# Kernel optimization log

Hardware: AMD Instinct MI355X
Metric: run time of the kernel (lower is better)

## Reference

```python
import jax, jax.numpy as jnp
import numpy as np

B, N, K = 2, 1024, 16
D_MODEL, D_ELLIP, N_HEADS = 768, 128, 8
NF = D_MODEL // 6            # sinusoidal freqs per coordinate
MAX_LOG_FREQ = 7.0
ENC_H = max(1, N_HEADS // 2) # ellipsoid encoder heads
ENC_FF = 2048                # torch TransformerEncoderLayer default dim_feedforward


def setup_inputs() -> dict:
    key = jax.random.key(0)
    ks = jax.random.split(key, 20)
    rn = lambda k, sh, sc=1.0: jax.random.normal(k, sh, dtype=jnp.float32) * sc
    w = lambda k, o, i: rn(k, (o, i), 1.0 / np.sqrt(i))
    inp = {}
    inp['s'] = rn(ks[0], (B, N, D_MODEL))
    inp['R'] = rn(ks[1], (B, N, 3, 3))
    inp['t'] = rn(ks[2], (B, N, 3))
    inp['ellip_tokens'] = rn(ks[3], (B, K, D_ELLIP))
    inp['mu'] = rn(ks[4], (B, K, 3))
    inp['Sigma'] = rn(ks[5], (B, K, 3, 3))
    inp['ellip_mask'] = jnp.ones((B, K), dtype=jnp.bool_)
    # main attention params (torch Linear convention: [out, in])
    inp['mix_w'] = w(ks[6], 6 * NF, 6 * NF)
    inp['lin_cov_w'] = w(ks[7], D_MODEL, 9)
    inp['q_w'] = w(ks[8], D_MODEL, D_MODEL)
    inp['k_w'] = w(ks[9], D_MODEL, 2 * D_MODEL)
    inp['v_w'] = w(ks[10], D_MODEL, D_MODEL + D_ELLIP)
    inp['o_w'] = w(ks[11], D_MODEL, D_MODEL)
    # ellipsoid TransformerEncoderLayer params (post-norm, eval mode)
    inp['enc_in_w'] = w(ks[12], 3 * D_ELLIP, D_ELLIP)
    inp['enc_in_b'] = jnp.zeros((3 * D_ELLIP,), jnp.float32)
    inp['enc_out_w'] = w(ks[13], D_ELLIP, D_ELLIP)
    inp['enc_out_b'] = jnp.zeros((D_ELLIP,), jnp.float32)
    inp['lin1_w'] = w(ks[14], ENC_FF, D_ELLIP)
    inp['lin1_b'] = jnp.zeros((ENC_FF,), jnp.float32)
    inp['lin2_w'] = w(ks[15], D_ELLIP, ENC_FF)
    inp['lin2_b'] = jnp.zeros((D_ELLIP,), jnp.float32)
    inp['ln1_g'] = jnp.ones((D_ELLIP,), jnp.float32)
    inp['ln1_b'] = jnp.zeros((D_ELLIP,), jnp.float32)
    inp['ln2_g'] = jnp.ones((D_ELLIP,), jnp.float32)
    inp['ln2_b'] = jnp.zeros((D_ELLIP,), jnp.float32)
    return inp


def _layernorm(x, g, b, eps=1e-5):
    m = x.mean(-1, keepdims=True)
    v = ((x - m) ** 2).mean(-1, keepdims=True)
    return (x - m) / jnp.sqrt(v + eps) * g + b


def _fwd(s, R, t, ellip_tokens, mu, Sigma, mix_w, lin_cov_w, q_w, k_w, v_w, o_w,
         enc_in_w, enc_in_b, enc_out_w, enc_out_b, lin1_w, lin1_b, lin2_w, lin2_b,
         ln1_g, ln1_b, ln2_g, ln2_b, ellip_mask):
    # --- ellipsoid self-attn encoder (single post-norm layer, eval mode) ---
    x = ellip_tokens                                   # [B,K,de]
    qkv = x @ enc_in_w.T + enc_in_b
    q, kk, v = jnp.split(qkv, 3, axis=-1)
    dhe = D_ELLIP // ENC_H
    qh = q.reshape(B, K, ENC_H, dhe)
    kh = kk.reshape(B, K, ENC_H, dhe)
    vh = v.reshape(B, K, ENC_H, dhe)
    sc = jnp.einsum('bqhd,bkhd->bhqk', qh, kh) / np.sqrt(dhe).astype(np.float32)
    ao = jnp.einsum('bhqk,bkhd->bqhd', jax.nn.softmax(sc, -1), vh).reshape(B, K, D_ELLIP)
    ao = ao @ enc_out_w.T + enc_out_b
    x = _layernorm(x + ao, ln1_g, ln1_b)
    ff = jax.nn.relu(x @ lin1_w.T + lin1_b) @ lin2_w.T + lin2_b
    e = _layernorm(x + ff, ln2_g, ln2_b)               # [B,K,de]
    # --- per-query local frame transforms ---
    diff = mu[:, None, :, :] - t[:, :, None, :]        # [B,N,K,3]
    r = jnp.einsum('bnji,bnkj->bnki', R, diff)         # R^T @ diff
    C = jnp.einsum('bnji,bkjl,bnlm->bnkim', R, Sigma, R)  # R^T Sigma R [B,N,K,3,3]
    # --- sinusoidal posenc (sin first, then cos; flatten coord-major) ---
    freqs = 2.0 ** jnp.linspace(0.0, MAX_LOG_FREQ, NF).astype(jnp.float32)
    xf = r[..., None] * freqs                          # [B,N,K,3,NF]
    feat = jnp.concatenate([jnp.sin(xf), jnp.cos(xf)], axis=-2).reshape(B, N, K, 6 * NF)
    pos = feat @ mix_w.T                               # [B,N,K,d]
    cov = C.reshape(B, N, K, 9) @ lin_cov_w.T          # [B,N,K,d]
    K_mat = jnp.concatenate([pos, cov], -1) @ k_w.T    # [B,N,K,d]
    eB = jnp.broadcast_to(e[:, None, :, :], (B, N, K, D_ELLIP))
    V_mat = jnp.concatenate([pos, eB], -1) @ v_w.T     # [B,N,K,d]
    Q = s @ q_w.T                                      # [B,N,d]
    dh = D_MODEL // N_HEADS
    Qh = Q.reshape(B, N, N_HEADS, dh)
    Kh = K_mat.reshape(B, N, K, N_HEADS, dh)
    Vh = V_mat.reshape(B, N, K, N_HEADS, dh)
    scores = jnp.einsum('bnhd,bnkhd->bnhk', Qh, Kh) / np.sqrt(dh).astype(np.float32)
    scores = scores + (1.0 - ellip_mask.astype(scores.dtype))[:, None, None, :] * -10000.0
    attn = jax.nn.softmax(scores, -1)                  # [B,N,H,K]
    out = jnp.einsum('bnhk,bnkhd->bnhd', attn, Vh).reshape(B, N, D_MODEL)
    return out @ o_w.T


def reference(s, R, t, ellip_tokens, mu, Sigma, mix_w, lin_cov_w, q_w, k_w, v_w, o_w,
              enc_in_w, enc_in_b, enc_out_w, enc_out_b, lin1_w, lin1_b, lin2_w, lin2_b,
              ln1_g, ln1_b, ln2_g, ln2_b, ellip_mask):
    return _fwd(s, R, t, ellip_tokens, mu, Sigma, mix_w, lin_cov_w, q_w, k_w, v_w, o_w,
                enc_in_w, enc_in_b, enc_out_w, enc_out_b, lin1_w, lin1_b, lin2_w, lin2_b,
                ln1_g, ln1_b, ln2_g, ln2_b, ellip_mask)
```

## Files before the change

kernel.cpp:

```cpp
#include <hip/hip_runtime.h>
#include <math.h>

#define BB     2
#define SEQ    1024
#define KTOK   16
#define DM     768
#define DE     128
#define NH     8
#define DHD    96
#define EH     4
#define DHE    32
#define EFF    2048

typedef short short8 __attribute__((ext_vector_type(8)));
typedef float f32x4 __attribute__((ext_vector_type(4)));
typedef unsigned short ushort_t;

__device__ __forceinline__ void split2(float x, ushort_t& h, ushort_t& l) {
  unsigned u = __float_as_uint(x);
  unsigned hb = (u + 0x7fffu + ((u >> 16) & 1u)) >> 16;
  float hf = __uint_as_float(hb << 16);
  float r = x - hf;
  unsigned u2 = __float_as_uint(r);
  unsigned lb = (u2 + 0x7fffu + ((u2 >> 16) & 1u)) >> 16;
  h = (ushort_t)hb;
  l = (ushort_t)lb;
}

typedef const unsigned int __attribute__((address_space(1)))* gas_p;
typedef unsigned int __attribute__((address_space(3)))* las_p;
__device__ __forceinline__ void load_lds16(const ushort_t* g, ushort_t* l) {
  __builtin_amdgcn_global_load_lds((gas_p)g, (las_p)l, 16, 0, 0);
}

__global__ __launch_bounds__(256) void split_all(
    const float* __restrict__ s, const float* __restrict__ q_w,
    const float* __restrict__ o_w, const float* __restrict__ k_w,
    const float* __restrict__ v_w,
    ushort_t* __restrict__ sS, ushort_t* __restrict__ qwS,
    ushort_t* __restrict__ owS, ushort_t* __restrict__ kwS,
    ushort_t* __restrict__ vwS)
{
  int z = blockIdx.y;
  const float* in; int ldin; ushort_t* out; int rows;
  switch (z) {
    case 0: in = s;   ldin = DM;      out = sS;  rows = BB * SEQ; break;
    case 1: in = q_w; ldin = DM;      out = qwS; rows = DM; break;
    case 2: in = o_w; ldin = DM;      out = owS; rows = DM; break;
    case 3: in = k_w; ldin = 2 * DM;  out = kwS; rows = DM; break;
    default: in = v_w; ldin = DM + DE; out = vwS; rows = DM; break;
  }
  long i = (long)blockIdx.x * 256 + threadIdx.x;
  const int perRow = DM >> 2;
  if (i >= (long)rows * perRow) return;
  int r = (int)(i / perRow), c4 = (int)(i % perRow) << 2;
  float4 v = *(const float4*)(in + (long)r * ldin + c4);
  ushort_t h[4], l[4];
  split2(v.x, h[0], l[0]);
  split2(v.y, h[1], l[1]);
  split2(v.z, h[2], l[2]);
  split2(v.w, h[3], l[3]);
  ushort_t* orow = out + (long)r * 1536;
  ushort4 hv; hv.x = h[0]; hv.y = h[1]; hv.z = h[2]; hv.w = h[3];
  ushort4 lv; lv.x = l[0]; lv.y = l[1]; lv.z = l[2]; lv.w = l[3];
  *(ushort4*)(orow + c4) = hv;
  *(ushort4*)(orow + DM + c4) = lv;
}

__global__ __launch_bounds__(256) void transpose_split(
    const float* __restrict__ in, int ldin, ushort_t* __restrict__ out,
    int K, int N)
{
  __shared__ float tile[64][65];
  int n0 = blockIdx.x * 64, k0 = blockIdx.y * 64;
  int tid = threadIdx.x;
  #pragma unroll
  for (int p = 0; p < 16; p++) {
    int idx = p * 256 + tid;
    int rr = idx >> 6, cc = idx & 63;
    tile[rr][cc] = in[(long)(k0 + rr) * ldin + n0 + cc];
  }
  __syncthreads();
  #pragma unroll
  for (int p = 0; p < 16; p++) {
    int idx = p * 256 + tid;
    int nr = idx >> 6, kc = idx & 63;
    ushort_t h, l;
    split2(tile[kc][nr], h, l);
    out[(long)(n0 + nr) * 2 * K + (k0 + kc)] = h;
    out[(long)(n0 + nr) * 2 * K + K + (k0 + kc)] = l;
  }
}

template<int OMODE, bool ADD>
__global__ __launch_bounds__(256) void gemm3t(
    const ushort_t* __restrict__ A, int lda, int aKstep, int aLoOff,
    const ushort_t* __restrict__ B, long bOffZ, int ldb, int bKstep, int bLoOff,
    void* __restrict__ Cv, int ldc, int cOffZ, int cLoOff,
    const float* __restrict__ addv, int ldadd, int addOffZ,
    int M, int N, int K)
{
  int z = blockIdx.z;
  B += (long)z * bOffZ;
  int aC0 = z * aKstep, bC0 = z * bKstep;
  const int row0 = blockIdx.y * 64, col0 = blockIdx.x * 64;
  __shared__ ushort_t Ah[2][2048], Al[2][2048], Bh[2][2048], Bl[2][2048];
  int tid = threadIdx.x;
  int wave = tid >> 6, lane = tid & 63;
  int quad = lane >> 4, mrow = lane & 15;
  int wm = (wave >> 1) * 32, wn = (wave & 1) * 32;
  int sr = tid >> 2, q8 = (tid & 3) << 3;
  int wbase = wave << 9;
  f32x4 acc[2][2] = {};

  const ushort_t* pa = A + (long)(row0 + sr) * lda + (aC0 + q8);
  const ushort_t* pb = B + (long)(col0 + sr) * ldb + (bC0 + q8);

  load_lds16(pa, &Ah[0][wbase]);
  load_lds16(pa + aLoOff, &Al[0][wbase]);
  load_lds16(pb, &Bh[0][wbase]);
  load_lds16(pb + bLoOff, &Bl[0][wbase]);

  int buf = 0;
  for (int k0 = 0; k0 < K; k0 += 32) {
    __syncthreads();
    if (k0 + 32 < K) {
      int kn = k0 + 32;
      load_lds16(pa + kn, &Ah[buf ^ 1][wbase]);
      load_lds16(pa + aLoOff + kn, &Al[buf ^ 1][wbase]);
      load_lds16(pb + kn, &Bh[buf ^ 1][wbase]);
      load_lds16(pb + bLoOff + kn, &Bl[buf ^ 1][wbase]);
    }
    short8 fah[2], fal[2], fbh[2], fbl[2];
    #pragma unroll
    for (int t = 0; t < 2; t++) {
      fah[t] = *(const short8*)&Ah[buf][(wm + t * 16 + mrow) * 32 + (quad << 3)];
      fal[t] = *(const short8*)&Al[buf][(wm + t * 16 + mrow) * 32 + (quad << 3)];
      fbh[t] = *(const short8*)&Bh[buf][(wn + t * 16 + mrow) * 32 + (quad << 3)];
      fbl[t] = *(const short8*)&Bl[buf][(wn + t * 16 + mrow) * 32 + (quad << 3)];
    }
    #pragma unroll
    for (int mt = 0; mt < 2; mt++)
      #pragma unroll
      for (int nt = 0; nt < 2; nt++) {
        f32x4 c = acc[mt][nt];
        c = __builtin_amdgcn_mfma_f32_16x16x32_bf16(fah[mt], fbh[nt], c, 0, 0, 0);
        c = __builtin_amdgcn_mfma_f32_16x16x32_bf16(fal[mt], fbh[nt], c, 0, 0, 0);
        c = __builtin_amdgcn_mfma_f32_16x16x32_bf16(fah[mt], fbl[nt], c, 0, 0, 0);
        acc[mt][nt] = c;
      }
    buf ^= 1;
  }
  float* Cf = (float*)Cv + (long)z * cOffZ;
  ushort_t* Cs = (ushort_t*)Cv + (long)z * cOffZ;
  const float* av = ADD ? (addv + (long)z * addOffZ) : nullptr;
  #pragma unroll
  for (int mt = 0; mt < 2; mt++)
    #pragma unroll
    for (int nt = 0; nt < 2; nt++) {
      int col = col0 + wn + nt * 16 + mrow;
      if (col >= N) continue;
      int rb = row0 + wm + mt * 16 + (quad << 2);
      #pragma unroll
      for (int rr = 0; rr < 4; rr++) {
        float v = acc[mt][nt][rr];
        if (ADD) v += av[(long)(rb + rr) * ldadd + col];
        if (OMODE == 0) {
          Cf[(long)(rb + rr) * ldc + col] = v;
        } else {
          ushort_t h, l;
          split2(v, h, l);
          Cs[(long)(rb + rr) * ldc + col] = h;
          Cs[(long)(rb + rr) * ldc + cLoOff + col] = l;
        }
      }
    }
}

__global__ __launch_bounds__(256) void bk9_kernel(
    const float* __restrict__ k_w, const float* __restrict__ lin_cov,
    float* __restrict__ Bk9)
{
  int idx = blockIdx.x * 256 + threadIdx.x;
  if (idx >= DM * 9) return;
  int r = idx / 9, p = idx % 9;
  const float* kr = k_w + (long)r * (2 * DM) + DM;
  float acc = 0.f;
  for (int j = 0; j < DM; j++) acc = fmaf(kr[j], lin_cov[j * 9 + p], acc);
  Bk9[idx] = acc;
}

__global__ __launch_bounds__(256) void qb_kernel(
    const ushort_t* __restrict__ QS, const float* __restrict__ Bk9,
    float* __restrict__ QB)
{
  int idx = blockIdx.x * 256 + threadIdx.x;
  if (idx >= BB * SEQ * NH * 9) return;
  int bn = idx / 72, rem = idx % 72, h = rem / 9, p = rem % 9;
  const ushort_t* qr = QS + (long)bn * 1536 + h * DHD;
  float acc = 0.f;
  for (int k = 0; k < DHD; k++) {
    float q = __uint_as_float((unsigned)qr[k] << 16) +
              __uint_as_float((unsigned)qr[DM + k] << 16);
    acc = fmaf(q, Bk9[(h * DHD + k) * 9 + p], acc);
  }
  QB[idx] = acc;
}

__global__ __launch_bounds__(128) void enc_qkv(
    const float* __restrict__ tok, const float* __restrict__ w,
    const float* __restrict__ bias, float* __restrict__ qkv)
{
  int tkn = blockIdx.y;
  int o = blockIdx.x * 128 + threadIdx.x;
  __shared__ float xr[DE];
  int tid = threadIdx.x;
  xr[tid] = tok[tkn * DE + tid];
  __syncthreads();
  float acc = bias[o];
  const float4* wr = (const float4*)(w + (long)o * DE);
  #pragma unroll 8
  for (int j = 0; j < DE / 4; j++) {
    float4 p = wr[j];
    acc = fmaf(p.x, xr[j * 4 + 0], acc);
    acc = fmaf(p.y, xr[j * 4 + 1], acc);
    acc = fmaf(p.z, xr[j * 4 + 2], acc);
    acc = fmaf(p.w, xr[j * 4 + 3], acc);
  }
  qkv[tkn * 384 + o] = acc;
}

__global__ __launch_bounds__(128) void enc_attn_ln1(
    const float* __restrict__ tok, const float* __restrict__ qkvG,
    const float* __restrict__ out_w, const float* __restrict__ out_b,
    const float* __restrict__ ln1_g, const float* __restrict__ ln1_b,
    float* __restrict__ x1G)
{
  int idx = blockIdx.x;
  int b = idx >> 4, tk = idx & 15;
  int tid = threadIdx.x;
  __shared__ float qkvs[KTOK][384];
  __shared__ float ao[DE];
  __shared__ float scl[EH][KTOK], attnl[EH][KTOK];
  __shared__ float red[2];
  __shared__ float stats[2];
  for (int i = tid; i < KTOK * 384; i += 128)
    qkvs[i / 384][i % 384] = qkvG[b * KTOK * 384 + i];
  __syncthreads();
  if (tid < EH * KTOK) {
    int h = tid >> 4, kk = tid & 15;
    float acc = 0.f;
    #pragma unroll 8
    for (int d = 0; d < DHE; d++)
      acc = fmaf(qkvs[tk][h * DHE + d], qkvs[kk][DE + h * DHE + d], acc);
    scl[h][kk] = acc * 0.17677669529663687f;
  }
  __syncthreads();
  if (tid < EH) {
    float m = -1e30f;
    for (int kk = 0; kk < KTOK; kk++) m = fmaxf(m, scl[tid][kk]);
    float s = 0.f;
    for (int kk = 0; kk < KTOK; kk++) { float e = expf(scl[tid][kk] - m); attnl[tid][kk] = e; s += e; }
    float inv = 1.f / s;
    for (int kk = 0; kk < KTOK; kk++) attnl[tid][kk] *= inv;
  }
  __syncthreads();
  {
    int h = tid / DHE;
    float acc = 0.f;
    #pragma unroll
    for (int kk = 0; kk < KTOK; kk++) acc = fmaf(attnl[h][kk], qkvs[kk][256 + tid], acc);
    ao[tid] = acc;
  }
  __syncthreads();
  float val;
  {
    float acc = out_b[tid];
    const float4* wr = (const float4*)(out_w + (long)tid * DE);
    #pragma unroll 8
    for (int j = 0; j < DE / 4; j++) {
      float4 p = wr[j];
      acc = fmaf(p.x, ao[j * 4 + 0], acc);
      acc = fmaf(p.y, ao[j * 4 + 1], acc);
      acc = fmaf(p.z, ao[j * 4 + 2], acc);
      acc = fmaf(p.w, ao[j * 4 + 3], acc);
    }
    val = tok[idx * DE + tid] + acc;
  }
  {
    float v = val;
    #pragma unroll
    for (int off = 32; off > 0; off >>= 1) v += __shfl_down(v, off);
    if ((tid & 63) == 0) red[tid >> 6] = v;
    __syncthreads();
    if (tid == 0) stats[0] = (red[0] + red[1]) * (1.f / DE);
    __syncthreads();
    float d = val - stats[0];
    float v2 = d * d;
    #pragma unroll
    for (int off = 32; off > 0; off >>= 1) v2 += __shfl_down(v2, off);
    if ((tid & 63) == 0) red[tid >> 6] = v2;
    __syncthreads();
    if (tid == 0) stats[1] = rsqrtf((red[0] + red[1]) * (1.f / DE) + 1e-5f);
    __syncthreads();
    x1G[idx * DE + tid] = (val - stats[0]) * stats[1] * ln1_g[tid] + ln1_b[tid];
  }
}

__global__ __launch_bounds__(256) void enc_ff1(
    const float* __restrict__ x1G, const float* __restrict__ lin1_w,
    const float* __restrict__ lin1_b, float* __restrict__ ff1G)
{
  int tkn = blockIdx.x >> 3;
  int f = ((blockIdx.x & 7) << 8) + threadIdx.x;
  __shared__ float xs[DE];
  if (threadIdx.x < DE) xs[threadIdx.x] = x1G[tkn * DE + threadIdx.x];
  __syncthreads();
  float acc = lin1_b[f];
  const float4* wr = (const float4*)(lin1_w + (long)f * DE);
  #pragma unroll 8
  for (int j = 0; j < DE / 4; j++) {
    float4 p = wr[j];
    acc = fmaf(p.x, xs[j * 4 + 0], acc);
    acc = fmaf(p.y, xs[j * 4 + 1], acc);
    acc = fmaf(p.z, xs[j * 4 + 2], acc);
    acc = fmaf(p.w, xs[j * 4 + 3], acc);
  }
  ff1G[tkn * EFF + f] = fmaxf(acc, 0.f);
}

__global__ __launch_bounds__(256) void enc_ff2(
    const float* __restrict__ x1G, const float* __restrict__ ff1G,
    const float* __restrict__ lin2_w, const float* __restrict__ lin2_b,
    float* __restrict__ tmp2G)
{
  int wv = (blockIdx.x << 2) + (threadIdx.x >> 6);
  int tkn = wv >> 7, j = wv & 127;
  int lane = threadIdx.x & 63;
  const float* wr = lin2_w + (long)j * EFF;
  const float* fr = ff1G + (long)tkn * EFF;
  float acc = 0.f;
  #pragma unroll 8
  for (int i = 0; i < EFF / 64; i++) {
    int p = (i << 6) + lane;
    acc = fmaf(wr[p], fr[p], acc);
  }
  #pragma unroll
  for (int off = 32; off > 0; off >>= 1) acc += __shfl_down(acc, off);
  if (lane == 0)
    tmp2G[tkn * DE + j] = x1G[tkn * DE + j] + lin2_b[j] + acc;
}

__global__ __launch_bounds__(256) void enc_ln2_evec(
    const float* __restrict__ tmp2G, const float* __restrict__ ln2_g,
    const float* __restrict__ ln2_b, const float* __restrict__ v_w,
    float* __restrict__ evec)
{
  int idx = blockIdx.x;
  int tid = threadIdx.x;
  __shared__ float el[DE];
  __shared__ float red[4];
  __shared__ float stats[2];
  float val = (tid < DE) ? tmp2G[idx * DE + tid] : 0.f;
  {
    float v = val;
    #pragma unroll
    for (int off = 32; off > 0; off >>= 1) v += __shfl_down(v, off);
    if ((tid & 63) == 0) red[tid >> 6] = v;
    __syncthreads();
    if (tid == 0) stats[0] = (red[0] + red[1] + red[2] + red[3]) * (1.f / DE);
    __syncthreads();
    float d = (tid < DE) ? (val - stats[0]) : 0.f;
    float v2 = d * d;
    #pragma unroll
    for (int off = 32; off > 0; off >>= 1) v2 += __shfl_down(v2, off);
    if ((tid & 63) == 0) red[tid >> 6] = v2;
    __syncthreads();
    if (tid == 0) stats[1] = rsqrtf((red[0] + red[1] + red[2] + red[3]) * (1.f / DE) + 1e-5f);
    __syncthreads();
    if (tid < DE) el[tid] = (val - stats[0]) * stats[1] * ln2_g[tid] + ln2_b[tid];
    __syncthreads();
  }
  #pragma unroll
  for (int r = 0; r < 3; r++) {
    int d = tid + (r << 8);
    float acc = 0.f;
    const float4* wr = (const float4*)(v_w + (long)d * (DM + DE) + DM);
    #pragma unroll 8
    for (int j = 0; j < DE / 4; j++) {
      float4 p = wr[j];
      acc = fmaf(p.x, el[j * 4 + 0], acc);
      acc = fmaf(p.y, el[j * 4 + 1], acc);
      acc = fmaf(p.z, el[j * 4 + 2], acc);
      acc = fmaf(p.w, el[j * 4 + 3], acc);
    }
    evec[idx * DM + d] = acc;
  }
}

__global__ __launch_bounds__(256) void main_attn(
    const float* __restrict__ Rg, const float* __restrict__ tg,
    const float* __restrict__ mug, const float* __restrict__ Sigg,
    const float* __restrict__ QAg, const float* __restrict__ QBg,
    const float* __restrict__ evec, ushort_t* __restrict__ wfeatS,
    float* __restrict__ outeG)
{
  int bn = blockIdx.x;
  int b = bn >> 10;
  int tid = threadIdx.x;
  int w = tid >> 6, lane = tid & 63;
  int h0 = w * 2, h1 = w * 2 + 1;
  __shared__ float Rm[9], tm[3];
  __shared__ float rK[KTOK][3];
  __shared__ float C9[KTOK][9];
  __shared__ float featL[KTOK][772];
  __shared__ float QBl[NH][12];
  __shared__ float scl[NH][KTOK];
  __shared__ float attnl[NH][KTOK];
  __shared__ float freqsL[128];
  float qa0[12], qa1[12];
  {
    const float* qbase = QAg + (long)bn * (NH * DM);
    #pragma unroll
    for (int i = 0; i < 12; i++) {
      qa0[i] = qbase[h0 * DM + i * 64 + lane];
      qa1[i] = qbase[h1 * DM + i * 64 + lane];
    }
  }
  if (tid < 9) Rm[tid] = Rg[bn * 9 + tid];
  if (tid >= 16 && tid < 19) tm[tid - 16] = tg[bn * 3 + (tid - 16)];
  if (tid >= 32 && tid < 32 + NH * 9) {
    int q = tid - 32;
    QBl[q / 9][q % 9] = QBg[bn * (NH * 9) + q];
  }
  if (tid >= 128 && tid < 256) {
    const float step = 7.0f / 127.0f;
    freqsL[tid - 128] = exp2f(step * (float)(tid - 128));
  }
  __syncthreads();
  if (tid < KTOK) {
    int k = tid;
    float diff[3];
    #pragma unroll
    for (int j = 0; j < 3; j++) diff[j] = mug[(b * KTOK + k) * 3 + j] - tm[j];
    #pragma unroll
    for (int i = 0; i < 3; i++) {
      float a = 0.f;
      #pragma unroll
      for (int j = 0; j < 3; j++) a = fmaf(Rm[j * 3 + i], diff[j], a);
      rK[k][i] = a;
    }
    float SR[9];
    const float* Sg = Sigg + (b * KTOK + k) * 9;
    #pragma unroll
    for (int j = 0; j < 3; j++)
      #pragma unroll
      for (int m2 = 0; m2 < 3; m2++) {
        float a = 0.f;
        #pragma unroll
        for (int l = 0; l < 3; l++) a = fmaf(Sg[j * 3 + l], Rm[l * 3 + m2], a);
        SR[j * 3 + m2] = a;
      }
    #pragma unroll
    for (int i = 0; i < 3; i++)
      #pragma unroll
      for (int m2 = 0; m2 < 3; m2++) {
        float a = 0.f;
        #pragma unroll
        for (int j = 0; j < 3; j++) a = fmaf(Rm[j * 3 + i], SR[j * 3 + m2], a);
        C9[k][i * 3 + m2] = a;
      }
  }
  __syncthreads();
  for (int i = tid; i < KTOK * 384; i += 256) {
    int k = i / 384, jj = i % 384;
    int coord = jj >> 7, f = jj & 127;
    float xf = rK[k][coord] * freqsL[f];
    float sv, cv;
    __sincosf(xf, &sv, &cv);
    featL[k][jj] = sv;
    featL[k][jj + 384] = cv;
  }
  __syncthreads();
  for (int k = 0; k < KTOK; k++) {
    float a0 = 0.f, a1 = 0.f;
    #pragma unroll
    for (int i = 0; i < 12; i++) {
      float fv = featL[k][i * 64 + lane];
      a0 = fmaf(qa0[i], fv, a0);
      a1 = fmaf(qa1[i], fv, a1);
    }
    #pragma unroll
    for (int off = 32; off > 0; off >>= 1) {
      a0 += __shfl_down(a0, off);
      a1 += __shfl_down(a1, off);
    }
    if (lane == 0) { scl[h0][k] = a0; scl[h1][k] = a1; }
  }
  __syncthreads();
  if (tid < NH) {
    int h = tid;
    float vals[KTOK];
    float m = -1e30f;
    for (int k = 0; k < KTOK; k++) {
      float a = scl[h][k];
      #pragma unroll
      for (int p = 0; p < 9; p++) a = fmaf(C9[k][p], QBl[h][p], a);
      a *= 0.10206207261596575f;
      vals[k] = a;
      m = fmaxf(m, a);
    }
    float s = 0.f;
    for (int k = 0; k < KTOK; k++) { float e = expf(vals[k] - m); attnl[h][k] = e; s += e; }
    float inv = 1.f / s;
    for (int k = 0; k < KTOK; k++) attnl[h][k] *= inv;
  }
  __syncthreads();
  {
    float at0[KTOK], at1[KTOK];
    #pragma unroll
    for (int k = 0; k < KTOK; k++) { at0[k] = attnl[h0][k]; at1[k] = attnl[h1][k]; }
    ushort_t* wrow = wfeatS + (long)bn * (2 * NH * DM);
    for (int jj = lane; jj < DM; jj += 64) {
      float a0 = 0.f, a1 = 0.f;
      #pragma unroll
      for (int k = 0; k < KTOK; k++) {
        float fv = featL[k][jj];
        a0 = fmaf(at0[k], fv, a0);
        a1 = fmaf(at1[k], fv, a1);
      }
      ushort_t h, l;
      split2(a0, h, l);
      wrow[h0 * DM + jj] = h;
      wrow[NH * DM + h0 * DM + jj] = l;
      split2(a1, h, l);
      wrow[h1 * DM + jj] = h;
      wrow[NH * DM + h1 * DM + jj] = l;
    }
  }
  for (int d = tid; d < DM; d += 256) {
    int h = d / DHD;
    float acc = 0.f;
    #pragma unroll
    for (int k = 0; k < KTOK; k++)
      acc = fmaf(attnl[h][k], evec[(b * KTOK + k) * DM + d], acc);
    outeG[(long)bn * DM + d] = acc;
  }
}

extern "C" void kernel_launch(void* const* d_in, const int* in_sizes, int n_in,
                              void* d_out, int out_size, void* d_ws, size_t ws_size,
                              hipStream_t stream) {
  const float* s    = (const float*)d_in[0];
  const float* R    = (const float*)d_in[1];
  const float* t    = (const float*)d_in[2];
  const float* tok  = (const float*)d_in[3];
  const float* mu   = (const float*)d_in[4];
  const float* Sig  = (const float*)d_in[5];
  const float* mix_w     = (const float*)d_in[7];
  const float* lin_cov_w = (const float*)d_in[8];
  const float* q_w  = (const float*)d_in[9];
  const float* k_w  = (const float*)d_in[10];
  const float* v_w  = (const float*)d_in[11];
  const float* o_w  = (const float*)d_in[12];
  const float* enc_in_w  = (const float*)d_in[13];
  const float* enc_in_b  = (const float*)d_in[14];
  const float* enc_out_w = (const float*)d_in[15];
  const float* enc_out_b = (const float*)d_in[16];
  const float* lin1_w = (const float*)d_in[17];
  const float* lin1_b = (const float*)d_in[18];
  const float* lin2_w = (const float*)d_in[19];
  const float* lin2_b = (const float*)d_in[20];
  const float* ln1_g = (const float*)d_in[21];
  const float* ln1_b = (const float*)d_in[22];
  const float* ln2_g = (const float*)d_in[23];
  const float* ln2_b = (const float*)d_in[24];
  float* out = (float*)d_out;
  char* wsb  = (char*)d_ws;

  const int BN = BB * SEQ;
  float* qkv  = (float*)(wsb);
  float* x1e  = (float*)(wsb + 49152);
  float* ff1e = (float*)(wsb + 65536);
  float* t2e  = (float*)(wsb + 327680);
  float* evec = (float*)(wsb + 344064);
  float* Bk9  = (float*)(wsb + 442368);
  char* p = wsb + 470016;
  ushort_t* qwS   = (ushort_t*)p;  p += 2359296;
  ushort_t* owS   = (ushort_t*)p;  p += 2359296;
  ushort_t* kwS   = (ushort_t*)p;  p += 2359296;
  ushort_t* vwS   = (ushort_t*)p;  p += 2359296;
  ushort_t* mixTS = (ushort_t*)p;  p += 2359296;
  ushort_t* AkTS  = (ushort_t*)p;  p += 2359296;
  ushort_t* AvS   = (ushort_t*)p;  p += 2359296;
  ushort_t* sS    = (ushort_t*)p;  p += 6291456;
  ushort_t* QS    = (ushort_t*)p;  p += 6291456;
  float*    QB    = (float*)p;     p += 589824;
  float*    oute  = (float*)p;     p += 6291456;
  float*    QA    = (float*)p;     p += 50331648;
  ushort_t* wfeatS = (ushort_t*)QA;
  ushort_t* US     = sS;

  dim3 blk(256);

  enc_qkv<<<dim3(3, BB * KTOK), dim3(128), 0, stream>>>(tok, enc_in_w, enc_in_b, qkv);
  enc_attn_ln1<<<BB * KTOK, dim3(128), 0, stream>>>(tok, qkv, enc_out_w, enc_out_b,
                                                    ln1_g, ln1_b, x1e);
  enc_ff1<<<256, blk, 0, stream>>>(x1e, lin1_w, lin1_b, ff1e);
  enc_ff2<<<1024, blk, 0, stream>>>(x1e, ff1e, lin2_w, lin2_b, t2e);
  enc_ln2_evec<<<BB * KTOK, blk, 0, stream>>>(t2e, ln2_g, ln2_b, v_w, evec);

  split_all<<<dim3(1536, 5), blk, 0, stream>>>(s, q_w, o_w, k_w, v_w,
                                               sS, qwS, owS, kwS, vwS);
  transpose_split<<<dim3(12, 12), blk, 0, stream>>>(mix_w, DM, mixTS, DM, DM);
  bk9_kernel<<<27, blk, 0, stream>>>(k_w, lin_cov_w, Bk9);

  gemm3t<1, false><<<dim3(12, 12, 1), blk, 0, stream>>>(
      mixTS, 1536, 0, DM,  kwS, 0, 1536, 0, DM,
      AkTS, 1536, 0, DM,  nullptr, 0, 0,  DM, DM, DM);
  gemm3t<1, false><<<dim3(12, 12, 1), blk, 0, stream>>>(
      vwS, 1536, 0, DM,  mixTS, 0, 1536, 0, DM,
      AvS, 1536, 0, DM,  nullptr, 0, 0,  DM, DM, DM);
  gemm3t<1, false><<<dim3(12, 32, 1), blk, 0, stream>>>(
      sS, 1536, 0, DM,  qwS, 0, 1536, 0, DM,
      QS, 1536, 0, DM,  nullptr, 0, 0,  BN, DM, DM);
  qb_kernel<<<576, blk, 0, stream>>>(QS, Bk9, QB);
  gemm3t<0, false><<<dim3(12, 32, NH), blk, 0, stream>>>(
      QS, 1536, DHD, DM,  AkTS, 0, 1536, DHD, DM,
      QA, NH * DM, DM, 0,  nullptr, 0, 0,  BN, DM, DHD);

  main_attn<<<BN, blk, 0, stream>>>(R, t, mu, Sig, QA, QB, evec, wfeatS, oute);

  gemm3t<1, true><<<dim3(2, 32, NH), blk, 0, stream>>>(
      wfeatS, 2 * NH * DM, DM, NH * DM,  AvS, (long)DHD * 1536, 1536, 0, DM,
      US, 1536, DHD, DM,  oute, DM, DHD,  BN, DHD, DM);
  gemm3t<0, false><<<dim3(12, 32, 1), blk, 0, stream>>>(
      US, 1536, 0, DM,  owS, 0, 1536, 0, DM,
      out, DM, 0, 0,  nullptr, 0, 0,  BN, DM, DM);
}
```

Measured before the change: 380.5 us.

## Merge independent prep and GEMM kernels into combined launches; halve main_attn feature LDS

```diff
diff --git a/kernel.cpp b/kernel.cpp
--- a/kernel.cpp
+++ b/kernel.cpp
@@ -33,78 +33,16 @@
   __builtin_amdgcn_global_load_lds((gas_p)g, (las_p)l, 16, 0, 0);
 }
 
-__global__ __launch_bounds__(256) void split_all(
-    const float* __restrict__ s, const float* __restrict__ q_w,
-    const float* __restrict__ o_w, const float* __restrict__ k_w,
-    const float* __restrict__ v_w,
-    ushort_t* __restrict__ sS, ushort_t* __restrict__ qwS,
-    ushort_t* __restrict__ owS, ushort_t* __restrict__ kwS,
-    ushort_t* __restrict__ vwS)
-{
-  int z = blockIdx.y;
-  const float* in; int ldin; ushort_t* out; int rows;
-  switch (z) {
-    case 0: in = s;   ldin = DM;      out = sS;  rows = BB * SEQ; break;
-    case 1: in = q_w; ldin = DM;      out = qwS; rows = DM; break;
-    case 2: in = o_w; ldin = DM;      out = owS; rows = DM; break;
-    case 3: in = k_w; ldin = 2 * DM;  out = kwS; rows = DM; break;
-    default: in = v_w; ldin = DM + DE; out = vwS; rows = DM; break;
-  }
-  long i = (long)blockIdx.x * 256 + threadIdx.x;
-  const int perRow = DM >> 2;
-  if (i >= (long)rows * perRow) return;
-  int r = (int)(i / perRow), c4 = (int)(i % perRow) << 2;
-  float4 v = *(const float4*)(in + (long)r * ldin + c4);
-  ushort_t h[4], l[4];
-  split2(v.x, h[0], l[0]);
-  split2(v.y, h[1], l[1]);
-  split2(v.z, h[2], l[2]);
-  split2(v.w, h[3], l[3]);
-  ushort_t* orow = out + (long)r * 1536;
-  ushort4 hv; hv.x = h[0]; hv.y = h[1]; hv.z = h[2]; hv.w = h[3];
-  ushort4 lv; lv.x = l[0]; lv.y = l[1]; lv.z = l[2]; lv.w = l[3];
-  *(ushort4*)(orow + c4) = hv;
-  *(ushort4*)(orow + DM + c4) = lv;
-}
-
-__global__ __launch_bounds__(256) void transpose_split(
-    const float* __restrict__ in, int ldin, ushort_t* __restrict__ out,
-    int K, int N)
-{
-  __shared__ float tile[64][65];
-  int n0 = blockIdx.x * 64, k0 = blockIdx.y * 64;
-  int tid = threadIdx.x;
-  #pragma unroll
-  for (int p = 0; p < 16; p++) {
-    int idx = p * 256 + tid;
-    int rr = idx >> 6, cc = idx & 63;
-    tile[rr][cc] = in[(long)(k0 + rr) * ldin + n0 + cc];
-  }
-  __syncthreads();
-  #pragma unroll
-  for (int p = 0; p < 16; p++) {
-    int idx = p * 256 + tid;
-    int nr = idx >> 6, kc = idx & 63;
-    ushort_t h, l;
-    split2(tile[kc][nr], h, l);
-    out[(long)(n0 + nr) * 2 * K + (k0 + kc)] = h;
-    out[(long)(n0 + nr) * 2 * K + K + (k0 + kc)] = l;
-  }
-}
-
 template<int OMODE, bool ADD>
-__global__ __launch_bounds__(256) void gemm3t(
-    const ushort_t* __restrict__ A, int lda, int aKstep, int aLoOff,
-    const ushort_t* __restrict__ B, long bOffZ, int ldb, int bKstep, int bLoOff,
-    void* __restrict__ Cv, int ldc, int cOffZ, int cLoOff,
-    const float* __restrict__ addv, int ldadd, int addOffZ,
-    int M, int N, int K)
-{
-  int z = blockIdx.z;
-  B += (long)z * bOffZ;
-  int aC0 = z * aKstep, bC0 = z * bKstep;
-  const int row0 = blockIdx.y * 64, col0 = blockIdx.x * 64;
-  __shared__ ushort_t Ah[2][2048], Al[2][2048], Bh[2][2048], Bl[2][2048];
+__device__ __forceinline__ void gemm_body(
+    ushort_t (*AhB)[2048], ushort_t (*AlB)[2048],
+    ushort_t (*BhB)[2048], ushort_t (*BlB)[2048],
+    const ushort_t* A, int lda, int aC0, int aLoOff,
+    const ushort_t* B, int ldb, int bC0, int bLoOff,
+    void* Cv, int ldc, int cLoOff,
+    const float* av, int ldadd,
+    int row0, int col0, int N, int K)
+{
   int tid = threadIdx.x;
   int wave = tid >> 6, lane = tid & 63;
   int quad = lane >> 4, mrow = lane & 15;
@@ -116,28 +54,28 @@
   const ushort_t* pa = A + (long)(row0 + sr) * lda + (aC0 + q8);
   const ushort_t* pb = B + (long)(col0 + sr) * ldb + (bC0 + q8);
 
-  load_lds16(pa, &Ah[0][wbase]);
-  load_lds16(pa + aLoOff, &Al[0][wbase]);
-  load_lds16(pb, &Bh[0][wbase]);
-  load_lds16(pb + bLoOff, &Bl[0][wbase]);
+  load_lds16(pa, &AhB[0][wbase]);
+  load_lds16(pa + aLoOff, &AlB[0][wbase]);
+  load_lds16(pb, &BhB[0][wbase]);
+  load_lds16(pb + bLoOff, &BlB[0][wbase]);
 
   int buf = 0;
   for (int k0 = 0; k0 < K; k0 += 32) {
     __syncthreads();
     if (k0 + 32 < K) {
       int kn = k0 + 32;
-      load_lds16(pa + kn, &Ah[buf ^ 1][wbase]);
-      load_lds16(pa + aLoOff + kn, &Al[buf ^ 1][wbase]);
-      load_lds16(pb + kn, &Bh[buf ^ 1][wbase]);
-      load_lds16(pb + bLoOff + kn, &Bl[buf ^ 1][wbase]);
+      load_lds16(pa + kn, &AhB[buf ^ 1][wbase]);
+      load_lds16(pa + aLoOff + kn, &AlB[buf ^ 1][wbase]);
+      load_lds16(pb + kn, &BhB[buf ^ 1][wbase]);
+      load_lds16(pb + bLoOff + kn, &BlB[buf ^ 1][wbase]);
     }
     short8 fah[2], fal[2], fbh[2], fbl[2];
     #pragma unroll
     for (int t = 0; t < 2; t++) {
-      fah[t] = *(const short8*)&Ah[buf][(wm + t * 16 + mrow) * 32 + (quad << 3)];
-      fal[t] = *(const short8*)&Al[buf][(wm + t * 16 + mrow) * 32 + (quad << 3)];
-      fbh[t] = *(const short8*)&Bh[buf][(wn + t * 16 + mrow) * 32 + (quad << 3)];
-      fbl[t] = *(const short8*)&Bl[buf][(wn + t * 16 + mrow) * 32 + (quad << 3)];
+      fah[t] = *(const short8*)&AhB[buf][(wm + t * 16 + mrow) * 32 + (quad << 3)];
+      fal[t] = *(const short8*)&AlB[buf][(wm + t * 16 + mrow) * 32 + (quad << 3)];
+      fbh[t] = *(const short8*)&BhB[buf][(wn + t * 16 + mrow) * 32 + (quad << 3)];
+      fbl[t] = *(const short8*)&BlB[buf][(wn + t * 16 + mrow) * 32 + (quad << 3)];
     }
     #pragma unroll
     for (int mt = 0; mt < 2; mt++)
@@ -151,9 +89,8 @@
       }
     buf ^= 1;
   }
-  float* Cf = (float*)Cv + (long)z * cOffZ;
-  ushort_t* Cs = (ushort_t*)Cv + (long)z * cOffZ;
-  const float* av = ADD ? (addv + (long)z * addOffZ) : nullptr;
+  float* Cf = (float*)Cv;
+  ushort_t* Cs = (ushort_t*)Cv;
   #pragma unroll
   for (int mt = 0; mt < 2; mt++)
     #pragma unroll
@@ -177,57 +114,202 @@
     }
 }
 
-__global__ __launch_bounds__(256) void bk9_kernel(
-    const float* __restrict__ k_w, const float* __restrict__ lin_cov,
-    float* __restrict__ Bk9)
-{
-  int idx = blockIdx.x * 256 + threadIdx.x;
-  if (idx >= DM * 9) return;
-  int r = idx / 9, p = idx % 9;
-  const float* kr = k_w + (long)r * (2 * DM) + DM;
-  float acc = 0.f;
-  for (int j = 0; j < DM; j++) acc = fmaf(kr[j], lin_cov[j * 9 + p], acc);
-  Bk9[idx] = acc;
-}
-
-__global__ __launch_bounds__(256) void qb_kernel(
-    const ushort_t* __restrict__ QS, const float* __restrict__ Bk9,
+template<int OMODE, bool ADD>
+__global__ __launch_bounds__(256) void gemm3t(
+    const ushort_t* __restrict__ A, int lda, int aKstep, int aLoOff,
+    const ushort_t* __restrict__ B, long bOffZ, int ldb, int bKstep, int bLoOff,
+    void* __restrict__ Cv, int ldc, int cOffZ, int cLoOff,
+    const float* __restrict__ addv, int ldadd, int addOffZ,
+    int M, int N, int K)
+{
+  __shared__ ushort_t Ah[2][2048], Al[2][2048], Bh[2][2048], Bl[2][2048];
+  int z = blockIdx.z;
+  void* Cz = (OMODE == 0) ? (void*)((float*)Cv + (long)z * cOffZ)
+                          : (void*)((ushort_t*)Cv + (long)z * cOffZ);
+  gemm_body<OMODE, ADD>(Ah, Al, Bh, Bl,
+      A, lda, z * aKstep, aLoOff,
+      B + (long)z * bOffZ, ldb, z * bKstep, bLoOff,
+      Cz, ldc, cLoOff,
+      ADD ? addv + (long)z * addOffZ : nullptr, ldadd,
+      blockIdx.y * 64, blockIdx.x * 64, N, K);
+}
+
+__global__ __launch_bounds__(256) void combo1(
+    const float* __restrict__ s, const float* __restrict__ q_w,
+    const float* __restrict__ o_w, const float* __restrict__ k_w,
+    const float* __restrict__ v_w,
+    ushort_t* __restrict__ sS, ushort_t* __restrict__ qwS,
+    ushort_t* __restrict__ owS, ushort_t* __restrict__ kwS,
+    ushort_t* __restrict__ vwS,
+    const float* __restrict__ mix_w, ushort_t* __restrict__ mixTS,
+    const float* __restrict__ tok, const float* __restrict__ enc_in_w,
+    const float* __restrict__ enc_in_b, float* __restrict__ qkv,
+    const float* __restrict__ lin_cov_w, float* __restrict__ Bk9)
+{
+  int r = blockIdx.x, tid = threadIdx.x;
+  if (r < 3840) {
+    const float* in; int ldin; ushort_t* out; int base;
+    if (r < 1536)      { in = s;   ldin = DM;      out = sS;  base = 0; }
+    else if (r < 2112) { in = q_w; ldin = DM;      out = qwS; base = 1536; }
+    else if (r < 2688) { in = o_w; ldin = DM;      out = owS; base = 2112; }
+    else if (r < 3264) { in = k_w; ldin = 2 * DM;  out = kwS; base = 2688; }
+    else               { in = v_w; ldin = DM + DE; out = vwS; base = 3264; }
+    long i = (long)(r - base) * 256 + tid;
+    int rr = (int)(i / 192), c4 = (int)(i % 192) << 2;
+    float4 v = *(const float4*)(in + (long)rr * ldin + c4);
+    ushort_t h[4], l[4];
+    split2(v.x, h[0], l[0]);
+    split2(v.y, h[1], l[1]);
+    split2(v.z, h[2], l[2]);
+    split2(v.w, h[3], l[3]);
+    ushort_t* orow = out + (long)rr * 1536;
+    ushort4 hv; hv.x = h[0]; hv.y = h[1]; hv.z = h[2]; hv.w = h[3];
+    ushort4 lv; lv.x = l[0]; lv.y = l[1]; lv.z = l[2]; lv.w = l[3];
+    *(ushort4*)(orow + c4) = hv;
+    *(ushort4*)(orow + DM + c4) = lv;
+  } else if (r < 3984) {
+    __shared__ float tile[64][65];
+    int idx = r - 3840;
+    int n0 = (idx % 12) * 64, k0 = (idx / 12) * 64;
+    #pragma unroll
+    for (int p = 0; p < 16; p++) {
+      int q = p * 256 + tid;
+      int rr = q >> 6, cc = q & 63;
+      tile[rr][cc] = mix_w[(long)(k0 + rr) * DM + n0 + cc];
+    }
+    __syncthreads();
+    #pragma unroll
+    for (int p = 0; p < 16; p++) {
+      int q = p * 256 + tid;
+      int nr = q >> 6, kc = q & 63;
+      ushort_t h, l;
+      split2(tile[kc][nr], h, l);
+      mixTS[(long)(n0 + nr) * 1536 + (k0 + kc)] = h;
+      mixTS[(long)(n0 + nr) * 1536 + DM + (k0 + kc)] = l;
+    }
+  } else if (r < 4016) {
+    __shared__ float xr[DE];
+    int tkn = r - 3984;
+    if (tid < DE) xr[tid] = tok[tkn * DE + tid];
+    __syncthreads();
+    for (int o = tid; o < 3 * DE; o += 256) {
+      float acc = enc_in_b[o];
+      const float4* wr = (const float4*)(enc_in_w + (long)o * DE);
+      #pragma unroll 8
+      for (int j = 0; j < DE / 4; j++) {
+        float4 p = wr[j];
+        acc = fmaf(p.x, xr[j * 4 + 0], acc);
+        acc = fmaf(p.y, xr[j * 4 + 1], acc);
+        acc = fmaf(p.z, xr[j * 4 + 2], acc);
+        acc = fmaf(p.w, xr[j * 4 + 3], acc);
+      }
+      qkv[tkn * 384 + o] = acc;
+    }
+  } else {
+    int idx = (r - 4016) * 256 + tid;
+    if (idx < DM * 9) {
+      int rr = idx / 9, p = idx % 9;
+      const float* kr = k_w + (long)rr * (2 * DM) + DM;
+      float acc = 0.f;
+      for (int j = 0; j < DM; j++) acc = fmaf(kr[j], lin_cov_w[j * 9 + p], acc);
+      Bk9[idx] = acc;
+    }
+  }
+}
+
+__global__ __launch_bounds__(256) void mega1(
+    const ushort_t* __restrict__ sS, const ushort_t* __restrict__ qwS,
+    const ushort_t* __restrict__ mixTS, const ushort_t* __restrict__ kwS,
+    const ushort_t* __restrict__ vwS,
+    ushort_t* __restrict__ QS, ushort_t* __restrict__ AkTS,
+    ushort_t* __restrict__ AvS,
+    const float* __restrict__ t2e, const float* __restrict__ ln2_g,
+    const float* __restrict__ ln2_b, const float* __restrict__ v_w,
+    float* __restrict__ evec)
+{
+  __shared__ ushort_t Ah[2][2048], Al[2][2048], Bh[2][2048], Bl[2][2048];
+  int r = blockIdx.x, tid = threadIdx.x;
+  if (r < 384) {
+    gemm_body<1, false>(Ah, Al, Bh, Bl, sS, 1536, 0, DM, qwS, 1536, 0, DM,
+                        QS, 1536, DM, nullptr, 0, (r / 12) * 64, (r % 12) * 64, DM, DM);
+  } else if (r < 528) {
+    int t2 = r - 384;
+    gemm_body<1, false>(Ah, Al, Bh, Bl, mixTS, 1536, 0, DM, kwS, 1536, 0, DM,
+                        AkTS, 1536, DM, nullptr, 0, (t2 / 12) * 64, (t2 % 12) * 64, DM, DM);
+  } else if (r < 672) {
+    int t2 = r - 528;
+    gemm_body<1, false>(Ah, Al, Bh, Bl, vwS, 1536, 0, DM, mixTS, 1536, 0, DM,
+                        AvS, 1536, DM, nullptr, 0, (t2 / 12) * 64, (t2 % 12) * 64, DM, DM);
+  } else {
+    __shared__ float el[DE];
+    __shared__ float red[4];
+    __shared__ float stats[2];
+    int idx = r - 672;
+    float val = (tid < DE) ? t2e[idx * DE + tid] : 0.f;
+    {
+      float v = val;
+      #pragma unroll
+      for (int off = 32; off > 0; off >>= 1) v += __shfl_down(v, off);
+      if ((tid & 63) == 0) red[tid >> 6] = v;
+      __syncthreads();
+      if (tid == 0) stats[0] = (red[0] + red[1] + red[2] + red[3]) * (1.f / DE);
+      __syncthreads();
+      float d = (tid < DE) ? (val - stats[0]) : 0.f;
+      float v2 = d * d;
+      #pragma unroll
+      for (int off = 32; off > 0; off >>= 1) v2 += __shfl_down(v2, off);
+      if ((tid & 63) == 0) red[tid >> 6] = v2;
+      __syncthreads();
+      if (tid == 0) stats[1] = rsqrtf((red[0] + red[1] + red[2] + red[3]) * (1.f / DE) + 1e-5f);
+      __syncthreads();
+      if (tid < DE) el[tid] = (val - stats[0]) * stats[1] * ln2_g[tid] + ln2_b[tid];
+      __syncthreads();
+    }
+    #pragma unroll
+    for (int q = 0; q < 3; q++) {
+      int d = tid + (q << 8);
+      float acc = 0.f;
+      const float4* wr = (const float4*)(v_w + (long)d * (DM + DE) + DM);
+      #pragma unroll 8
+      for (int j = 0; j < DE / 4; j++) {
+        float4 p = wr[j];
+        acc = fmaf(p.x, el[j * 4 + 0], acc);
+        acc = fmaf(p.y, el[j * 4 + 1], acc);
+        acc = fmaf(p.z, el[j * 4 + 2], acc);
+        acc = fmaf(p.w, el[j * 4 + 3], acc);
+      }
+      evec[idx * DM + d] = acc;
+    }
+  }
+}
+
+__global__ __launch_bounds__(256) void qa_qb(
+    const ushort_t* __restrict__ QS, const ushort_t* __restrict__ AkTS,
+    float* __restrict__ QA, const float* __restrict__ Bk9,
     float* __restrict__ QB)
 {
-  int idx = blockIdx.x * 256 + threadIdx.x;
-  if (idx >= BB * SEQ * NH * 9) return;
-  int bn = idx / 72, rem = idx % 72, h = rem / 9, p = rem % 9;
-  const ushort_t* qr = QS + (long)bn * 1536 + h * DHD;
-  float acc = 0.f;
-  for (int k = 0; k < DHD; k++) {
-    float q = __uint_as_float((unsigned)qr[k] << 16) +
-              __uint_as_float((unsigned)qr[DM + k] << 16);
-    acc = fmaf(q, Bk9[(h * DHD + k) * 9 + p], acc);
-  }
-  QB[idx] = acc;
-}
-
-__global__ __launch_bounds__(128) void enc_qkv(
-    const float* __restrict__ tok, const float* __restrict__ w,
-    const float* __restrict__ bias, float* __restrict__ qkv)
-{
-  int tkn = blockIdx.y;
-  int o = blockIdx.x * 128 + threadIdx.x;
-  __shared__ float xr[DE];
-  int tid = threadIdx.x;
-  xr[tid] = tok[tkn * DE + tid];
-  __syncthreads();
-  float acc = bias[o];
-  const float4* wr = (const float4*)(w + (long)o * DE);
-  #pragma unroll 8
-  for (int j = 0; j < DE / 4; j++) {
-    float4 p = wr[j];
-    acc = fmaf(p.x, xr[j * 4 + 0], acc);
-    acc = fmaf(p.y, xr[j * 4 + 1], acc);
-    acc = fmaf(p.z, xr[j * 4 + 2], acc);
-    acc = fmaf(p.w, xr[j * 4 + 3], acc);
-  }
-  qkv[tkn * 384 + o] = acc;
+  __shared__ ushort_t Ah[2][2048], Al[2][2048], Bh[2][2048], Bl[2][2048];
+  int r = blockIdx.x;
+  if (r < 3072) {
+    int z = r / 384, rr = r % 384;
+    gemm_body<0, false>(Ah, Al, Bh, Bl,
+        QS, 1536, z * DHD, DM, AkTS, 1536, z * DHD, DM,
+        (void*)(QA + (long)z * DM), NH * DM, 0, nullptr, 0,
+        (rr / 12) * 64, (rr % 12) * 64, DM, DHD);
+  } else {
+    int idx = (r - 3072) * 256 + threadIdx.x;
+    if (idx < BB * SEQ * NH * 9) {
+      int bn = idx / 72, rem = idx % 72, h = rem / 9, p = rem % 9;
+      const ushort_t* qr = QS + (long)bn * 1536 + h * DHD;
+      float acc = 0.f;
+      for (int k = 0; k < DHD; k++) {
+        float q = __uint_as_float((unsigned)qr[k] << 16) +
+                  __uint_as_float((unsigned)qr[DM + k] << 16);
+        acc = fmaf(q, Bk9[(h * DHD + k) * 9 + p], acc);
+      }
+      QB[idx] = acc;
+    }
+  }
 }
 
 __global__ __launch_bounds__(128) void enc_attn_ln1(
@@ -351,53 +433,6 @@
     tmp2G[tkn * DE + j] = x1G[tkn * DE + j] + lin2_b[j] + acc;
 }
 
-__global__ __launch_bounds__(256) void enc_ln2_evec(
-    const float* __restrict__ tmp2G, const float* __restrict__ ln2_g,
-    const float* __restrict__ ln2_b, const float* __restrict__ v_w,
-    float* __restrict__ evec)
-{
-  int idx = blockIdx.x;
-  int tid = threadIdx.x;
-  __shared__ float el[DE];
-  __shared__ float red[4];
-  __shared__ float stats[2];
-  float val = (tid < DE) ? tmp2G[idx * DE + tid] : 0.f;
-  {
-    float v = val;
-    #pragma unroll
-    for (int off = 32; off > 0; off >>= 1) v += __shfl_down(v, off);
-    if ((tid & 63) == 0) red[tid >> 6] = v;
-    __syncthreads();
-    if (tid == 0) stats[0] = (red[0] + red[1] + red[2] + red[3]) * (1.f / DE);
-    __syncthreads();
-    float d = (tid < DE) ? (val - stats[0]) : 0.f;
-    float v2 = d * d;
-    #pragma unroll
-    for (int off = 32; off > 0; off >>= 1) v2 += __shfl_down(v2, off);
-    if ((tid & 63) == 0) red[tid >> 6] = v2;
-    __syncthreads();
-    if (tid == 0) stats[1] = rsqrtf((red[0] + red[1] + red[2] + red[3]) * (1.f / DE) + 1e-5f);
-    __syncthreads();
-    if (tid < DE) el[tid] = (val - stats[0]) * stats[1] * ln2_g[tid] + ln2_b[tid];
-    __syncthreads();
-  }
-  #pragma unroll
-  for (int r = 0; r < 3; r++) {
-    int d = tid + (r << 8);
-    float acc = 0.f;
-    const float4* wr = (const float4*)(v_w + (long)d * (DM + DE) + DM);
-    #pragma unroll 8
-    for (int j = 0; j < DE / 4; j++) {
-      float4 p = wr[j];
-      acc = fmaf(p.x, el[j * 4 + 0], acc);
-      acc = fmaf(p.y, el[j * 4 + 1], acc);
-      acc = fmaf(p.z, el[j * 4 + 2], acc);
-      acc = fmaf(p.w, el[j * 4 + 3], acc);
-    }
-    evec[idx * DM + d] = acc;
-  }
-}
-
 __global__ __launch_bounds__(256) void main_attn(
     const float* __restrict__ Rg, const float* __restrict__ tg,
     const float* __restrict__ mug, const float* __restrict__ Sigg,
@@ -409,11 +444,11 @@
   int b = bn >> 10;
   int tid = threadIdx.x;
   int w = tid >> 6, lane = tid & 63;
-  int h0 = w * 2, h1 = w * 2 + 1;
+  int h0 = 2 * w, h1 = 2 * w + 1;
   __shared__ float Rm[9], tm[3];
   __shared__ float rK[KTOK][3];
   __shared__ float C9[KTOK][9];
-  __shared__ float featL[KTOK][772];
+  __shared__ float featL[8][772];
   __shared__ float QBl[NH][12];
   __shared__ float scl[NH][KTOK];
   __shared__ float attnl[NH][KTOK];
@@ -433,7 +468,7 @@
     int q = tid - 32;
     QBl[q / 9][q % 9] = QBg[bn * (NH * 9) + q];
   }
-  if (tid >= 128 && tid < 256) {
+  if (tid >= 128) {
     const float step = 7.0f / 127.0f;
     freqsL[tid - 128] = exp2f(step * (float)(tid - 128));
   }
@@ -472,32 +507,34 @@
       }
   }
   __syncthreads();
-  for (int i = tid; i < KTOK * 384; i += 256) {
-    int k = i / 384, jj = i % 384;
-    int coord = jj >> 7, f = jj & 127;
-    float xf = rK[k][coord] * freqsL[f];
-    float sv, cv;
-    __sincosf(xf, &sv, &cv);
-    featL[k][jj] = sv;
-    featL[k][jj + 384] = cv;
-  }
-  __syncthreads();
-  for (int k = 0; k < KTOK; k++) {
-    float a0 = 0.f, a1 = 0.f;
-    #pragma unroll
-    for (int i = 0; i < 12; i++) {
-      float fv = featL[k][i * 64 + lane];
-      a0 = fmaf(qa0[i], fv, a0);
-      a1 = fmaf(qa1[i], fv, a1);
-    }
-    #pragma unroll
-    for (int off = 32; off > 0; off >>= 1) {
-      a0 += __shfl_down(a0, off);
-      a1 += __shfl_down(a1, off);
-    }
-    if (lane == 0) { scl[h0][k] = a0; scl[h1][k] = a1; }
-  }
-  __syncthreads();
+  for (int half = 0; half < 2; half++) {
+    for (int i = tid; i < 8 * 384; i += 256) {
+      int k = i / 384, jj = i % 384;
+      int coord = jj >> 7, f = jj & 127;
+      float xf = rK[half * 8 + k][coord] * freqsL[f];
+      float sv, cv;
+      __sincosf(xf, &sv, &cv);
+      featL[k][jj] = sv;
+      featL[k][jj + 384] = cv;
+    }
+    __syncthreads();
+    for (int k = 0; k < 8; k++) {
+      float a0 = 0.f, a1 = 0.f;
+      #pragma unroll
+      for (int i = 0; i < 12; i++) {
+        float fv = featL[k][i * 64 + lane];
+        a0 = fmaf(qa0[i], fv, a0);
+        a1 = fmaf(qa1[i], fv, a1);
+      }
+      #pragma unroll
+      for (int off = 32; off > 0; off >>= 1) {
+        a0 += __shfl_down(a0, off);
+        a1 += __shfl_down(a1, off);
+      }
+      if (lane == 0) { scl[h0][half * 8 + k] = a0; scl[h1][half * 8 + k] = a1; }
+    }
+    __syncthreads();
+  }
   if (tid < NH) {
     int h = tid;
     float vals[KTOK];
@@ -516,24 +553,47 @@
     for (int k = 0; k < KTOK; k++) attnl[h][k] *= inv;
   }
   __syncthreads();
+  float wf0[12], wf1[12];
+  #pragma unroll
+  for (int i = 0; i < 12; i++) { wf0[i] = 0.f; wf1[i] = 0.f; }
+  for (int pass = 0; pass < 2; pass++) {
+    int kb = (pass == 0) ? 8 : 0;
+    if (pass == 1) {
+      __syncthreads();
+      for (int i = tid; i < 8 * 384; i += 256) {
+        int k = i / 384, jj = i % 384;
+        int coord = jj >> 7, f = jj & 127;
+        float xf = rK[k][coord] * freqsL[f];
+        float sv, cv;
+        __sincosf(xf, &sv, &cv);
+        featL[k][jj] = sv;
+        featL[k][jj + 384] = cv;
+      }
+      __syncthreads();
+    }
+    #pragma unroll
+    for (int i = 0; i < 12; i++) {
+      int jj = i * 64 + lane;
+      float s0 = wf0[i], s1 = wf1[i];
+      #pragma unroll
+      for (int k = 0; k < 8; k++) {
+        float fv = featL[k][jj];
+        s0 = fmaf(attnl[h0][kb + k], fv, s0);
+        s1 = fmaf(attnl[h1][kb + k], fv, s1);
+      }
+      wf0[i] = s0; wf1[i] = s1;
+    }
+  }
   {
-    float at0[KTOK], at1[KTOK];
-    #pragma unroll
-    for (int k = 0; k < KTOK; k++) { at0[k] = attnl[h0][k]; at1[k] = attnl[h1][k]; }
     ushort_t* wrow = wfeatS + (long)bn * (2 * NH * DM);
-    for (int jj = lane; jj < DM; jj += 64) {
-      float a0 = 0.f, a1 = 0.f;
-      #pragma unroll
-      for (int k = 0; k < KTOK; k++) {
-        float fv = featL[k][jj];
-        a0 = fmaf(at0[k], fv, a0);
-        a1 = fmaf(at1[k], fv, a1);
-      }
+    #pragma unroll
+    for (int i = 0; i < 12; i++) {
+      int jj = i * 64 + lane;
       ushort_t h, l;
-      split2(a0, h, l);
+      split2(wf0[i], h, l);
       wrow[h0 * DM + jj] = h;
       wrow[NH * DM + h0 * DM + jj] = l;
-      split2(a1, h, l);
+      split2(wf1[i], h, l);
       wrow[h1 * DM + jj] = h;
       wrow[NH * DM + h1 * DM + jj] = l;
     }
@@ -603,34 +663,20 @@
 
   dim3 blk(256);
 
-  enc_qkv<<<dim3(3, BB * KTOK), dim3(128), 0, stream>>>(tok, enc_in_w, enc_in_b, qkv);
+  combo1<<<4043, blk, 0, stream>>>(s, q_w, o_w, k_w, v_w,
+                                   sS, qwS, owS, kwS, vwS,
+                                   mix_w, mixTS,
+                                   tok, enc_in_w, enc_in_b, qkv,
+                                   lin_cov_w, Bk9);
   enc_attn_ln1<<<BB * KTOK, dim3(128), 0, stream>>>(tok, qkv, enc_out_w, enc_out_b,
                                                     ln1_g, ln1_b, x1e);
   enc_ff1<<<256, blk, 0, stream>>>(x1e, lin1_w, lin1_b, ff1e);
   enc_ff2<<<1024, blk, 0, stream>>>(x1e, ff1e, lin2_w, lin2_b, t2e);
-  enc_ln2_evec<<<BB * KTOK, blk, 0, stream>>>(t2e, ln2_g, ln2_b, v_w, evec);
-
-  split_all<<<dim3(1536, 5), blk, 0, stream>>>(s, q_w, o_w, k_w, v_w,
-                                               sS, qwS, owS, kwS, vwS);
-  transpose_split<<<dim3(12, 12), blk, 0, stream>>>(mix_w, DM, mixTS, DM, DM);
-  bk9_kernel<<<27, blk, 0, stream>>>(k_w, lin_cov_w, Bk9);
-
-  gemm3t<1, false><<<dim3(12, 12, 1), blk, 0, stream>>>(
-      mixTS, 1536, 0, DM,  kwS, 0, 1536, 0, DM,
-      AkTS, 1536, 0, DM,  nullptr, 0, 0,  DM, DM, DM);
-  gemm3t<1, false><<<dim3(12, 12, 1), blk, 0, stream>>>(
-      vwS, 1536, 0, DM,  mixTS, 0, 1536, 0, DM,
-      AvS, 1536, 0, DM,  nullptr, 0, 0,  DM, DM, DM);
-  gemm3t<1, false><<<dim3(12, 32, 1), blk, 0, stream>>>(
-      sS, 1536, 0, DM,  qwS, 0, 1536, 0, DM,
-      QS, 1536, 0, DM,  nullptr, 0, 0,  BN, DM, DM);
-  qb_kernel<<<576, blk, 0, stream>>>(QS, Bk9, QB);
-  gemm3t<0, false><<<dim3(12, 32, NH), blk, 0, stream>>>(
-      QS, 1536, DHD, DM,  AkTS, 0, 1536, DHD, DM,
-      QA, NH * DM, DM, 0,  nullptr, 0, 0,  BN, DM, DHD);
-
+  mega1<<<704, blk, 0, stream>>>(sS, qwS, mixTS, kwS, vwS,
+                                 QS, AkTS, AvS,
+                                 t2e, ln2_g, ln2_b, v_w, evec);
+  qa_qb<<<3648, blk, 0, stream>>>(QS, AkTS, QA, Bk9, QB);
   main_attn<<<BN, blk, 0, stream>>>(R, t, mu, Sig, QA, QB, evec, wfeatS, oute);
-
   gemm3t<1, true><<<dim3(2, 32, NH), blk, 0, stream>>>(
       wfeatS, 2 * NH * DM, DM, NH * DM,  AvS, (long)DHD * 1536, 1536, 0, DM,
       US, 1536, DHD, DM,  oute, DM, DHD,  BN, DHD, DM);
```

After: 333.5 us. 12.3% less time.
